# Optimization experiments

Hardware: AMD Instinct MI355X
Metric: run time of the kernel (lower is better)

The kernel has to match this reference:

```python
import jax, jax.numpy as jnp
import numpy as np

H = 8
D_MODEL = 1024
DIM_G = 64
WAVE_LEN = 1000.0


def box_relational_embedding(f_g):
    # f_g: [B, N, 4] -> [B, N, N, 64] trigonometric geometry embedding
    B, N, _ = f_g.shape
    x_min, y_min, x_max, y_max = jnp.split(f_g, 4, axis=-1)  # each [B, N, 1]
    cx = (x_min + x_max) * 0.5
    cy = (y_min + y_max) * 0.5
    w = x_max - x_min + 1.0
    h = y_max - y_min + 1.0
    # row i vs column j deltas, normalized by row box size
    dx = jnp.log(jnp.maximum(jnp.abs((cx - cx.reshape(B, 1, N)) / w), 1e-3))
    dy = jnp.log(jnp.maximum(jnp.abs((cy - cy.reshape(B, 1, N)) / h), 1e-3))
    dw = jnp.log(w / w.reshape(B, 1, N))
    dh = jnp.log(h / h.reshape(B, 1, N))
    pos = jnp.stack([dx, dy, dw, dh], axis=-1)  # [B, N, N, 4]
    feat_range = jnp.arange(DIM_G // 8, dtype=jnp.float32) / (DIM_G / 8.0)
    dim_mat = 1.0 / jnp.power(WAVE_LEN, feat_range)  # [8]
    mul = (100.0 * pos)[..., None] * dim_mat  # [B, N, N, 4, 8]
    mul = mul.reshape(B, N, N, DIM_G // 2)
    return jnp.concatenate([jnp.sin(mul), jnp.cos(mul)], axis=-1)  # [B, N, N, 64]


def setup_inputs() -> dict:
    key = jax.random.key(0)
    ks = jax.random.split(key, 12)
    B, N, D = 16, 256, D_MODEL
    q = jax.random.normal(ks[0], (B, N, D), jnp.float32)
    k = jax.random.normal(ks[1], (B, N, D), jnp.float32)
    v = jax.random.normal(ks[2], (B, N, D), jnp.float32)
    # valid boxes: x_max > x_min, y_max > y_min
    xy = jax.random.uniform(ks[3], (B, N, 2), jnp.float32) * 100.0
    wh = jax.random.uniform(ks[4], (B, N, 2), jnp.float32) * 50.0 + 1.0
    input_box = jnp.concatenate([xy, xy + wh], axis=-1)  # [B, N, 4]
    s = 0.02
    Wq = jax.random.normal(ks[5], (D, D), jnp.float32) * s
    Wk = jax.random.normal(ks[6], (D, D), jnp.float32) * s
    Wv = jax.random.normal(ks[7], (D, D), jnp.float32) * s
    Wo = jax.random.normal(ks[8], (D, D), jnp.float32) * s
    bq = jnp.zeros((D,), jnp.float32)
    bk = jnp.zeros((D,), jnp.float32)
    bv = jnp.zeros((D,), jnp.float32)
    bo = jnp.zeros((D,), jnp.float32)
    Wg = jax.random.normal(ks[9], (H, DIM_G), jnp.float32) * 0.1  # stacked per-head Linear(64,1)
    bg = jax.random.normal(ks[10], (H,), jnp.float32) * 0.1
    return {"input_query": q, "input_key": k, "input_value": v, "input_box": input_box,
            "Wq": Wq, "bq": bq, "Wk": Wk, "bk": bk, "Wv": Wv, "bv": bv,
            "Wg": Wg, "bg": bg, "Wo": Wo, "bo": bo}


def reference(input_query, input_key, input_value, input_box,
              Wq, bq, Wk, bk, Wv, bv, Wg, bg, Wo, bo):
    B, N, D = input_query.shape
    d_k = D // H

    def proj(x, W, b):
        return (x @ W + b).reshape(B, N, H, d_k).transpose(0, 2, 1, 3)  # [B,H,N,dk]

    q = proj(input_query, Wq, bq)
    k = proj(input_key, Wk, bk)
    v = proj(input_value, Wv, bv)

    emb = box_relational_embedding(input_box)  # [B, N, N, 64]
    # per-head Linear(64 -> 1), stacked: [B, H, N, N]
    rel_w = jax.nn.relu(jnp.einsum('bmng,hg->bhmn', emb, Wg) + bg[None, :, None, None])

    scores = jnp.einsum('bhqd,bhkd->bhqk', q, k) / np.sqrt(d_k).astype(np.float32)
    logits = jnp.log(jnp.maximum(rel_w, 1e-6)) + scores
    attn = jax.nn.softmax(logits, axis=-1)  # [B, H, N, N]
    out = jnp.einsum('bhqk,bhkd->bhqd', attn, v)
    out = out.transpose(0, 2, 1, 3).reshape(B, N, D)
    return out @ Wo + bo
```

## Files before the change

### kernel.cpp

```cpp
#include <hip/hip_runtime.h>
#include <hip/hip_bf16.h>
#include <hip/hip_fp16.h>
#include <math.h>

#define B_  16
#define N_  256
#define D_  1024
#define H_  8
#define DK_ 128

typedef unsigned short u16;
typedef __attribute__((ext_vector_type(8))) short s8v;
typedef __attribute__((ext_vector_type(4))) float f4v;

__device__ __forceinline__ u16 f2b(float x) {
    union { float f; unsigned u; } v; v.f = x;
    unsigned r = v.u + 0x7fffu + ((v.u >> 16) & 1u);
    return (u16)(r >> 16);
}

__device__ __forceinline__ void gload16(void* lds, const void* g) {
    __builtin_amdgcn_global_load_lds(
        (const __attribute__((address_space(1))) void*)g,
        (__attribute__((address_space(3))) void*)lds, 16, 0, 0);
}

__device__ __forceinline__ void waitv8() { asm volatile("s_waitcnt vmcnt(8)" ::: "memory"); }
__device__ __forceinline__ void waitv6() { asm volatile("s_waitcnt vmcnt(6)" ::: "memory"); }
__device__ __forceinline__ void waitv4() { asm volatile("s_waitcnt vmcnt(4)" ::: "memory"); }
__device__ __forceinline__ void waitv3() { asm volatile("s_waitcnt vmcnt(3)" ::: "memory"); }
__device__ __forceinline__ void waitv0() { asm volatile("s_waitcnt vmcnt(0)" ::: "memory"); }
__device__ __forceinline__ void membar() { asm volatile("" ::: "memory"); }

__global__ __launch_bounds__(256)
void cvt_kernel(const float* __restrict__ x0, const float* __restrict__ x1,
                const float* __restrict__ x2, u16* __restrict__ out)
{
    const float* in = (blockIdx.y == 0) ? x0 : (blockIdx.y == 1) ? x1 : x2;
    u16* o = out + (size_t)blockIdx.y * 4194304;
    const int i = blockIdx.x * 256 + threadIdx.x;
    const float4 a = ((const float4*)in)[2 * i];
    const float4 b = ((const float4*)in)[2 * i + 1];
    union { u16 s[8]; uint4 v; } t;
    t.s[0] = f2b(a.x); t.s[1] = f2b(a.y); t.s[2] = f2b(a.z); t.s[3] = f2b(a.w);
    t.s[4] = f2b(b.x); t.s[5] = f2b(b.y); t.s[6] = f2b(b.z); t.s[7] = f2b(b.w);
    ((uint4*)o)[i] = t.v;
}

__global__ __launch_bounds__(256)
void cvtT_kernel(const float* __restrict__ W0, const float* __restrict__ W1,
                 const float* __restrict__ W2, const float* __restrict__ W3,
                 u16* __restrict__ out)
{
    const float* W = (blockIdx.z == 0) ? W0 : (blockIdx.z == 1) ? W1 :
                     (blockIdx.z == 2) ? W2 : W3;
    u16* o = out + (size_t)blockIdx.z * (D_ * D_);
    __shared__ float t[32][33];
    const int k0 = blockIdx.x * 32, n0 = blockIdx.y * 32;
    const int c = threadIdx.x & 31, r8 = threadIdx.x >> 5;
#pragma unroll
    for (int rr = 0; rr < 4; ++rr)
        t[r8 + rr * 8][c] = W[(size_t)(k0 + r8 + rr * 8) * D_ + n0 + c];
    __syncthreads();
#pragma unroll
    for (int rr = 0; rr < 4; ++rr)
        o[(size_t)(n0 + r8 + rr * 8) * D_ + k0 + c] = f2b(t[c][r8 + rr * 8]);
}

template<int BM, int FM, int LOADS, int MODE>
__global__ __launch_bounds__(256)
void gemm_kernel(const u16* __restrict__ A0, const u16* __restrict__ Wt0,
                 const float* __restrict__ b0, const float* __restrict__ b1,
                 const float* __restrict__ b2, void* __restrict__ outb)
{
    constexpr int WM  = FM * 16;
    constexpr int MT8 = (4096 / BM) / 8;
    __shared__ __align__(16) u16 As[3][BM][32];
    __shared__ __align__(16) u16 Bs[3][128][32];

    const int z = blockIdx.z;
    const u16* A  = A0  + (size_t)z * 4194304;
    const u16* Wt = Wt0 + (size_t)z * 1048576;
    const float* bias = (z == 0) ? b0 : (z == 1) ? b1 : b2;

    const int bid = blockIdx.x;
    const int xcd = bid & 7;
    const int wic = bid >> 3;
    const int by  = xcd * MT8 + (wic & (MT8 - 1));
    const int bx  = wic / MT8;
    const int m0  = by * BM;
    const int n0  = bx * 128;

    const int tid  = threadIdx.x;
    const int lane = tid & 63;
    const int w    = tid >> 6;
    const int l15  = lane & 15;
    const int l4   = lane >> 4;
    const int wr   = w >> 1;
    const int wc   = w & 1;

    const int gr   = tid >> 2;
    const int c4   = tid & 3;
    const int scol = (c4 ^ ((gr >> 1) & 3)) * 8;
    const int doff = c4 * 8;
    const u16* asrc = A  + (size_t)(m0 + gr) * 1024 + scol;
    const u16* bsrc = Wt + (size_t)(n0 + gr) * 1024 + scol;
    const int fc = (l4 ^ ((l15 >> 1) & 3)) * 8;

    auto stage = [&](int buf, int kt) {
        const int k0_ = kt * 32;
        gload16(&As[buf][gr][doff], asrc + k0_);
        if constexpr (BM == 128)
            gload16(&As[buf][gr + 64][doff], asrc + 64 * 1024 + k0_);
        gload16(&Bs[buf][gr][doff], bsrc + k0_);
        gload16(&Bs[buf][gr + 64][doff], bsrc + 64 * 1024 + k0_);
    };

    f4v acc[FM][4] = {};

    stage(0, 0);
    stage(1, 1);
    int cur = 0, stg = 2;

    for (int kt = 0; kt < 32; ++kt) {
        membar();
        __builtin_amdgcn_s_barrier();
        if (kt < 30) {
            stage(stg, kt + 2);
            if constexpr (LOADS == 4) waitv8(); else waitv6();
        } else if (kt == 30) {
            if constexpr (LOADS == 4) waitv4(); else waitv3();
        } else {
            waitv0();
        }
        membar();
        __builtin_amdgcn_s_barrier();

        s8v af[FM], bf[4];
#pragma unroll
        for (int i = 0; i < FM; ++i)
            af[i] = *(const s8v*)&As[cur][wr * WM + i * 16 + l15][fc];
#pragma unroll
        for (int j = 0; j < 4; ++j)
            bf[j] = *(const s8v*)&Bs[cur][wc * 64 + j * 16 + l15][fc];
#pragma unroll
        for (int i = 0; i < FM; ++i)
#pragma unroll
            for (int j = 0; j < 4; ++j)
                acc[i][j] = __builtin_amdgcn_mfma_f32_16x16x32_bf16(
                    af[i], bf[j], acc[i][j], 0, 0, 0);

        cur = (cur == 2) ? 0 : cur + 1;
        stg = (stg == 2) ? 0 : stg + 1;
    }

#pragma unroll
    for (int j = 0; j < 4; ++j) {
        const int n = n0 + wc * 64 + j * 16 + l15;
        const float bb = bias[n];
#pragma unroll
        for (int i = 0; i < FM; ++i) {
            const int mbase = m0 + wr * WM + i * 16 + l4 * 4;
            if constexpr (MODE == 0) {
#pragma unroll
                for (int reg = 0; reg < 4; ++reg)
                    ((float*)outb)[(size_t)(mbase + reg) * 1024 + n] =
                        acc[i][j][reg] + bb;
            } else {
                if (z == 2) {
                    const int b = mbase >> 8, tok = mbase & 255;
                    const int h = n >> 7, d = n & 127;
                    ushort4 st;
                    st.x = f2b(acc[i][j][0] + bb);
                    st.y = f2b(acc[i][j][1] + bb);
                    st.z = f2b(acc[i][j][2] + bb);
                    st.w = f2b(acc[i][j][3] + bb);
                    *(ushort4*)&((u16*)outb)[(size_t)z * 4194304 +
                        (((size_t)b * H_ + h) * DK_ + d) * N_ + tok] = st;
                } else {
                    const int h = n >> 7, d = n & 127;
#pragma unroll
                    for (int reg = 0; reg < 4; ++reg) {
                        const int m = mbase + reg;
                        const int b = m >> 8, tok = m & 255;
                        ((u16*)outb)[(size_t)z * 4194304 +
                            (((size_t)b * H_ + h) * N_ + tok) * DK_ + d] =
                            f2b(acc[i][j][reg] + bb);
                    }
                }
            }
        }
    }
}

__global__ __launch_bounds__(256)
void boxbias_kernel(const float* __restrict__ fg, const float* __restrict__ Wg,
                    const float* __restrict__ bg, _Float16* __restrict__ lb)
{
    __shared__ float sWg[512];
    __shared__ float sbg[8];
    const int tid = threadIdx.x;
    const int b = blockIdx.x >> 8;
    const int i = blockIdx.x & 255;

    sWg[tid] = Wg[tid];
    sWg[tid + 256] = Wg[tid + 256];
    if (tid < 8) sbg[tid] = bg[tid];

    const float4 bi = *(const float4*)&fg[(size_t)(b * N_ + i) * 4];
    const float cxi = 0.5f * (bi.x + bi.z);
    const float cyi = 0.5f * (bi.y + bi.w);
    const float wi  = bi.z - bi.x + 1.0f;
    const float hi  = bi.w - bi.y + 1.0f;

    const int j = tid;
    const float4 bj = *(const float4*)&fg[(size_t)(b * N_ + j) * 4];
    const float cxj = 0.5f * (bj.x + bj.z);
    const float cyj = 0.5f * (bj.y + bj.w);
    const float wj  = bj.z - bj.x + 1.0f;
    const float hj  = bj.w - bj.y + 1.0f;

    const float pos[4] = {
        logf(fmaxf(fabsf((cxi - cxj) / wi), 1e-3f)) * 100.0f,
        logf(fmaxf(fabsf((cyi - cyj) / hi), 1e-3f)) * 100.0f,
        logf(wi / wj) * 100.0f,
        logf(hi / hj) * 100.0f
    };
    const float dim[8] = {1.0f, 0.421696503f, 0.177827941f, 0.0749894209f,
                          0.0316227766f, 0.0133352143f, 0.00562341325f, 0.00237137371f};

    float sv[32], cv[32];
#pragma unroll
    for (int p = 0; p < 4; ++p)
#pragma unroll
        for (int q = 0; q < 8; ++q)
            __sincosf(pos[p] * dim[q], &sv[p * 8 + q], &cv[p * 8 + q]);

    __syncthreads();
#pragma unroll
    for (int h = 0; h < 8; ++h) {
        float acc = sbg[h];
        const float* wrow = &sWg[h * 64];
#pragma unroll
        for (int g = 0; g < 32; ++g)
            acc = fmaf(sv[g], wrow[g], fmaf(cv[g], wrow[32 + g], acc));
        const float rel = fmaxf(acc, 0.0f);
        lb[(((size_t)b * H_ + h) * N_ + i) * N_ + j] =
            (_Float16)logf(fmaxf(rel, 1e-6f));
    }
}

__global__ __launch_bounds__(256)
void attn_mfma_kernel(const u16* __restrict__ qp, const u16* __restrict__ kp,
                      const u16* __restrict__ vp, const _Float16* __restrict__ lb,
                      u16* __restrict__ ao)
{
    __shared__ __align__(16) u16 Ks[32][136];
    __shared__ __align__(16) u16 Vt[128][40];
    __shared__ __align__(16) u16 Ps[4][32][40];

    const int tid  = threadIdx.x;
    const int lane = tid & 63;
    const int w    = tid >> 6;
    const int l15  = lane & 15;
    const int l4   = lane >> 4;
    const int bh   = blockIdx.x >> 1;
    const int qt   = blockIdx.x & 1;
    const int q0   = qt * 128 + w * 32;

    s8v qf[2][4];
    const u16* qb = qp + ((size_t)bh * N_ + q0) * DK_;
#pragma unroll
    for (int mf = 0; mf < 2; ++mf)
#pragma unroll
        for (int ks = 0; ks < 4; ++ks)
            qf[mf][ks] = *(const s8v*)(qb + (size_t)(mf * 16 + l15) * DK_ + ks * 32 + l4 * 8);

    f4v o[2][8] = {};
    float m_r[2][4], l_r[2][4];
#pragma unroll
    for (int mf = 0; mf < 2; ++mf)
#pragma unroll
        for (int r = 0; r < 4; ++r) { m_r[mf][r] = -INFINITY; l_r[mf][r] = 0.0f; }

    const float scale = 0.08838834764831845f;
    const _Float16* lbb = lb + ((size_t)bh * N_ + q0) * N_;

    const int sr = tid >> 3;
    const int sc = (tid & 7) * 16;
    const int vr = tid >> 2;
    const int vs = (tid & 3) * 8;

    for (int kt = 0; kt < 8; ++kt) {
        __syncthreads();
        {
            const u16* ksrc = kp + ((size_t)bh * N_ + kt * 32) * DK_;
            *(s8v*)&Ks[sr][sc]     = *(const s8v*)(ksrc + (size_t)sr * DK_ + sc);
            *(s8v*)&Ks[sr][sc + 8] = *(const s8v*)(ksrc + (size_t)sr * DK_ + sc + 8);
        }
        {
            const u16* vsrc = vp + ((size_t)bh * DK_ + vr) * N_ + kt * 32 + vs;
            const s8v v0 = *(const s8v*)vsrc;
            const s8v v1 = *(const s8v*)(vsrc + 64 * N_);
            *(s8v*)&Vt[vr][vs]      = v0;
            *(s8v*)&Vt[vr + 64][vs] = v1;
        }
        __syncthreads();

        f4v s[2][2] = {};
#pragma unroll
        for (int ks = 0; ks < 4; ++ks) {
#pragma unroll
            for (int kf = 0; kf < 2; ++kf) {
                const s8v kb = *(const s8v*)&Ks[kf * 16 + l15][ks * 32 + l4 * 8];
#pragma unroll
                for (int mf = 0; mf < 2; ++mf)
                    s[mf][kf] = __builtin_amdgcn_mfma_f32_16x16x32_bf16(
                        qf[mf][ks], kb, s[mf][kf], 0, 0, 0);
            }
        }
#pragma unroll
        for (int mf = 0; mf < 2; ++mf)
#pragma unroll
            for (int kf = 0; kf < 2; ++kf)
#pragma unroll
                for (int r = 0; r < 4; ++r)
                    s[mf][kf][r] = fmaf(s[mf][kf][r], scale, (float)
                        lbb[(size_t)(mf * 16 + l4 * 4 + r) * N_ + kt * 32 + kf * 16 + l15]);

#pragma unroll
        for (int mf = 0; mf < 2; ++mf) {
            float rm[4], al[4];
#pragma unroll
            for (int r = 0; r < 4; ++r) rm[r] = fmaxf(s[mf][0][r], s[mf][1][r]);
#pragma unroll
            for (int st = 1; st <= 8; st <<= 1)
#pragma unroll
                for (int r = 0; r < 4; ++r) rm[r] = fmaxf(rm[r], __shfl_xor(rm[r], st));
#pragma unroll
            for (int r = 0; r < 4; ++r) {
                const float mn = fmaxf(m_r[mf][r], rm[r]);
                al[r] = __expf(m_r[mf][r] - mn);
                m_r[mf][r] = mn;
            }
            float p0[4], p1[4], rs[4];
#pragma unroll
            for (int r = 0; r < 4; ++r) {
                p0[r] = __expf(s[mf][0][r] - m_r[mf][r]);
                p1[r] = __expf(s[mf][1][r] - m_r[mf][r]);
                rs[r] = p0[r] + p1[r];
            }
#pragma unroll
            for (int st = 1; st <= 8; st <<= 1)
#pragma unroll
                for (int r = 0; r < 4; ++r) rs[r] += __shfl_xor(rs[r], st);
#pragma unroll
            for (int r = 0; r < 4; ++r) {
                l_r[mf][r] = l_r[mf][r] * al[r] + rs[r];
                Ps[w][mf * 16 + l4 * 4 + r][l15]      = f2b(p0[r]);
                Ps[w][mf * 16 + l4 * 4 + r][16 + l15] = f2b(p1[r]);
            }
#pragma unroll
            for (int nf = 0; nf < 8; ++nf)
#pragma unroll
                for (int r = 0; r < 4; ++r) o[mf][nf][r] *= al[r];
        }

        s8v pa[2];
#pragma unroll
        for (int mf = 0; mf < 2; ++mf)
            pa[mf] = *(const s8v*)&Ps[w][mf * 16 + l15][l4 * 8];
#pragma unroll
        for (int nf = 0; nf < 8; ++nf) {
            const s8v vb = *(const s8v*)&Vt[nf * 16 + l15][l4 * 8];
#pragma unroll
            for (int mf = 0; mf < 2; ++mf)
                o[mf][nf] = __builtin_amdgcn_mfma_f32_16x16x32_bf16(
                    pa[mf], vb, o[mf][nf], 0, 0, 0);
        }
    }

    const int b = bh >> 3, h = bh & 7;
#pragma unroll
    for (int mf = 0; mf < 2; ++mf) {
        float inv[4];
#pragma unroll
        for (int r = 0; r < 4; ++r) inv[r] = 1.0f / l_r[mf][r];
#pragma unroll
        for (int nf = 0; nf < 8; ++nf) {
#pragma unroll
            for (int r = 0; r < 4; ++r) {
                const int tok = q0 + mf * 16 + l4 * 4 + r;
                const int d = nf * 16 + l15;
                ao[(((size_t)b * N_ + tok) * H_ + h) * DK_ + d] = f2b(o[mf][nf][r] * inv[r]);
            }
        }
    }
}

extern "C" void kernel_launch(void* const* d_in, const int* in_sizes, int n_in,
                              void* d_out, int out_size, void* d_ws, size_t ws_size,
                              hipStream_t stream)
{
    const float* xq = (const float*)d_in[0];
    const float* xk = (const float*)d_in[1];
    const float* xv = (const float*)d_in[2];
    const float* fg = (const float*)d_in[3];
    const float* Wq = (const float*)d_in[4];
    const float* bq = (const float*)d_in[5];
    const float* Wk = (const float*)d_in[6];
    const float* bk = (const float*)d_in[7];
    const float* Wv = (const float*)d_in[8];
    const float* bv = (const float*)d_in[9];
    const float* Wg = (const float*)d_in[10];
    const float* bg = (const float*)d_in[11];
    const float* Wo = (const float*)d_in[12];
    const float* bo = (const float*)d_in[13];

    char* w8 = (char*)d_ws;
    u16*      xb  = (u16*)(w8);
    u16*      Wt  = (u16*)(w8 + 25165824);
    u16*      qkv = (u16*)(w8 + 33554432);
    _Float16* lb  = (_Float16*)(w8 + 58720256);
    u16*      ao  = (u16*)(w8 + 75497472);

    cvt_kernel<<<dim3(2048, 3), 256, 0, stream>>>(xq, xk, xv, xb);
    cvtT_kernel<<<dim3(32, 32, 4), 256, 0, stream>>>(Wq, Wk, Wv, Wo, Wt);

    gemm_kernel<128, 4, 4, 1><<<dim3(256, 1, 3), 256, 0, stream>>>(
        xb, Wt, bq, bk, bv, qkv);

    boxbias_kernel<<<B_ * N_, 256, 0, stream>>>(fg, Wg, bg, lb);

    attn_mfma_kernel<<<B_ * H_ * 2, 256, 0, stream>>>(
        qkv, qkv + 4194304, qkv + 2 * 4194304, lb, ao);

    gemm_kernel<64, 2, 3, 0><<<dim3(512, 1, 1), 256, 0, stream>>>(
        ao, Wt + 3 * 1048576, bo, bo, bo, d_out);
}
```

Baseline: 128.3 us.

## Merge prep and box-bias launches, split attention into 64-row query tiles

```diff
diff --git a/kernel.cpp b/kernel.cpp
--- a/kernel.cpp
+++ b/kernel.cpp
@@ -33,140 +33,136 @@
 __device__ __forceinline__ void membar() { asm volatile("" ::: "memory"); }
 
 __global__ __launch_bounds__(256)
-void cvt_kernel(const float* __restrict__ x0, const float* __restrict__ x1,
-                const float* __restrict__ x2, u16* __restrict__ out)
+void prep_kernel(const float* __restrict__ x0, const float* __restrict__ x1,
+                 const float* __restrict__ x2,
+                 const float* __restrict__ W0, const float* __restrict__ W1,
+                 const float* __restrict__ W2, const float* __restrict__ W3,
+                 u16* __restrict__ xb, u16* __restrict__ Wt)
 {
-    const float* in = (blockIdx.y == 0) ? x0 : (blockIdx.y == 1) ? x1 : x2;
-    u16* o = out + (size_t)blockIdx.y * 4194304;
-    const int i = blockIdx.x * 256 + threadIdx.x;
-    const float4 a = ((const float4*)in)[2 * i];
-    const float4 b = ((const float4*)in)[2 * i + 1];
-    union { u16 s[8]; uint4 v; } t;
-    t.s[0] = f2b(a.x); t.s[1] = f2b(a.y); t.s[2] = f2b(a.z); t.s[3] = f2b(a.w);
-    t.s[4] = f2b(b.x); t.s[5] = f2b(b.y); t.s[6] = f2b(b.z); t.s[7] = f2b(b.w);
-    ((uint4*)o)[i] = t.v;
+    const int bx = blockIdx.x;
+    if (bx < 6144) {
+        const int y = bx >> 11;
+        const float* in = (y == 0) ? x0 : (y == 1) ? x1 : x2;
+        u16* o = xb + (size_t)y * 4194304;
+        const int i = (bx & 2047) * 256 + threadIdx.x;
+        const float4 a = ((const float4*)in)[2 * i];
+        const float4 b = ((const float4*)in)[2 * i + 1];
+        union { u16 s[8]; uint4 v; } t;
+        t.s[0] = f2b(a.x); t.s[1] = f2b(a.y); t.s[2] = f2b(a.z); t.s[3] = f2b(a.w);
+        t.s[4] = f2b(b.x); t.s[5] = f2b(b.y); t.s[6] = f2b(b.z); t.s[7] = f2b(b.w);
+        ((uint4*)o)[i] = t.v;
+    } else {
+        __shared__ float t[32][33];
+        const int tt = bx - 6144;
+        const int z  = tt >> 10;
+        const int rem = tt & 1023;
+        const int k0 = (rem & 31) * 32;
+        const int n0 = (rem >> 5) * 32;
+        const float* W = (z == 0) ? W0 : (z == 1) ? W1 : (z == 2) ? W2 : W3;
+        u16* o = Wt + (size_t)z * (D_ * D_);
+        const int c = threadIdx.x & 31, r8 = threadIdx.x >> 5;
+#pragma unroll
+        for (int rr = 0; rr < 4; ++rr)
+            t[r8 + rr * 8][c] = W[(size_t)(k0 + r8 + rr * 8) * D_ + n0 + c];
+        __syncthreads();
+#pragma unroll
+        for (int rr = 0; rr < 4; ++rr)
+            o[(size_t)(n0 + r8 + rr * 8) * D_ + k0 + c] = f2b(t[c][r8 + rr * 8]);
+    }
 }
 
 __global__ __launch_bounds__(256)
-void cvtT_kernel(const float* __restrict__ W0, const float* __restrict__ W1,
-                 const float* __restrict__ W2, const float* __restrict__ W3,
-                 u16* __restrict__ out)
+void qkv_boxbias_kernel(const u16* __restrict__ A0, const u16* __restrict__ Wt0,
+                        const float* __restrict__ b0, const float* __restrict__ b1,
+                        const float* __restrict__ b2, u16* __restrict__ qkv,
+                        const float* __restrict__ fg, const float* __restrict__ Wg,
+                        const float* __restrict__ bg, _Float16* __restrict__ lb)
 {
-    const float* W = (blockIdx.z == 0) ? W0 : (blockIdx.z == 1) ? W1 :
-                     (blockIdx.z == 2) ? W2 : W3;
-    u16* o = out + (size_t)blockIdx.z * (D_ * D_);
-    __shared__ float t[32][33];
-    const int k0 = blockIdx.x * 32, n0 = blockIdx.y * 32;
-    const int c = threadIdx.x & 31, r8 = threadIdx.x >> 5;
-#pragma unroll
-    for (int rr = 0; rr < 4; ++rr)
-        t[r8 + rr * 8][c] = W[(size_t)(k0 + r8 + rr * 8) * D_ + n0 + c];
-    __syncthreads();
-#pragma unroll
-    for (int rr = 0; rr < 4; ++rr)
-        o[(size_t)(n0 + r8 + rr * 8) * D_ + k0 + c] = f2b(t[c][r8 + rr * 8]);
-}
-
-template<int BM, int FM, int LOADS, int MODE>
-__global__ __launch_bounds__(256)
-void gemm_kernel(const u16* __restrict__ A0, const u16* __restrict__ Wt0,
-                 const float* __restrict__ b0, const float* __restrict__ b1,
-                 const float* __restrict__ b2, void* __restrict__ outb)
-{
-    constexpr int WM  = FM * 16;
-    constexpr int MT8 = (4096 / BM) / 8;
-    __shared__ __align__(16) u16 As[3][BM][32];
+    __shared__ __align__(16) u16 As[3][128][32];
     __shared__ __align__(16) u16 Bs[3][128][32];
-
-    const int z = blockIdx.z;
-    const u16* A  = A0  + (size_t)z * 4194304;
-    const u16* Wt = Wt0 + (size_t)z * 1048576;
-    const float* bias = (z == 0) ? b0 : (z == 1) ? b1 : b2;
-
-    const int bid = blockIdx.x;
-    const int xcd = bid & 7;
-    const int wic = bid >> 3;
-    const int by  = xcd * MT8 + (wic & (MT8 - 1));
-    const int bx  = wic / MT8;
-    const int m0  = by * BM;
-    const int n0  = bx * 128;
-
-    const int tid  = threadIdx.x;
-    const int lane = tid & 63;
-    const int w    = tid >> 6;
-    const int l15  = lane & 15;
-    const int l4   = lane >> 4;
-    const int wr   = w >> 1;
-    const int wc   = w & 1;
-
-    const int gr   = tid >> 2;
-    const int c4   = tid & 3;
-    const int scol = (c4 ^ ((gr >> 1) & 3)) * 8;
-    const int doff = c4 * 8;
-    const u16* asrc = A  + (size_t)(m0 + gr) * 1024 + scol;
-    const u16* bsrc = Wt + (size_t)(n0 + gr) * 1024 + scol;
-    const int fc = (l4 ^ ((l15 >> 1) & 3)) * 8;
-
-    auto stage = [&](int buf, int kt) {
-        const int k0_ = kt * 32;
-        gload16(&As[buf][gr][doff], asrc + k0_);
-        if constexpr (BM == 128)
+    __shared__ float sWg[512];
+    __shared__ float sbg[8];
+
+    const int tid = threadIdx.x;
+
+    if (blockIdx.x < 768) {
+        const int gbx = blockIdx.x;
+        const int z   = gbx >> 8;
+        const int bid = gbx & 255;
+        const u16* A  = A0  + (size_t)z * 4194304;
+        const u16* Wt = Wt0 + (size_t)z * 1048576;
+        const float* bias = (z == 0) ? b0 : (z == 1) ? b1 : b2;
+
+        const int xcd = bid & 7;
+        const int wic = bid >> 3;
+        const int by  = xcd * 4 + (wic & 3);
+        const int bx_ = wic >> 2;
+        const int m0  = by * 128;
+        const int n0  = bx_ * 128;
+
+        const int lane = tid & 63;
+        const int w    = tid >> 6;
+        const int l15  = lane & 15;
+        const int l4   = lane >> 4;
+        const int wr   = w >> 1;
+        const int wc   = w & 1;
+
+        const int gr   = tid >> 2;
+        const int c4   = tid & 3;
+        const int scol = (c4 ^ ((gr >> 1) & 3)) * 8;
+        const int doff = c4 * 8;
+        const u16* asrc = A  + (size_t)(m0 + gr) * 1024 + scol;
+        const u16* bsrc = Wt + (size_t)(n0 + gr) * 1024 + scol;
+        const int fc = (l4 ^ ((l15 >> 1) & 3)) * 8;
+
+        auto stage = [&](int buf, int kt) {
+            const int k0_ = kt * 32;
+            gload16(&As[buf][gr][doff],      asrc + k0_);
             gload16(&As[buf][gr + 64][doff], asrc + 64 * 1024 + k0_);
-        gload16(&Bs[buf][gr][doff], bsrc + k0_);
-        gload16(&Bs[buf][gr + 64][doff], bsrc + 64 * 1024 + k0_);
-    };
-
-    f4v acc[FM][4] = {};
-
-    stage(0, 0);
-    stage(1, 1);
-    int cur = 0, stg = 2;
-
-    for (int kt = 0; kt < 32; ++kt) {
-        membar();
-        __builtin_amdgcn_s_barrier();
-        if (kt < 30) {
-            stage(stg, kt + 2);
-            if constexpr (LOADS == 4) waitv8(); else waitv6();
-        } else if (kt == 30) {
-            if constexpr (LOADS == 4) waitv4(); else waitv3();
-        } else {
-            waitv0();
-        }
-        membar();
-        __builtin_amdgcn_s_barrier();
-
-        s8v af[FM], bf[4];
-#pragma unroll
-        for (int i = 0; i < FM; ++i)
-            af[i] = *(const s8v*)&As[cur][wr * WM + i * 16 + l15][fc];
-#pragma unroll
-        for (int j = 0; j < 4; ++j)
-            bf[j] = *(const s8v*)&Bs[cur][wc * 64 + j * 16 + l15][fc];
-#pragma unroll
-        for (int i = 0; i < FM; ++i)
+            gload16(&Bs[buf][gr][doff],      bsrc + k0_);
+            gload16(&Bs[buf][gr + 64][doff], bsrc + 64 * 1024 + k0_);
+        };
+
+        f4v acc[4][4] = {};
+
+        stage(0, 0);
+        stage(1, 1);
+        int cur = 0, stg = 2;
+
+        for (int kt = 0; kt < 32; ++kt) {
+            membar();
+            __builtin_amdgcn_s_barrier();
+            if (kt < 30) { stage(stg, kt + 2); waitv8(); }
+            else if (kt == 30) { waitv4(); }
+            else { waitv0(); }
+            membar();
+            __builtin_amdgcn_s_barrier();
+
+            s8v af[4], bf[4];
+#pragma unroll
+            for (int i = 0; i < 4; ++i)
+                af[i] = *(const s8v*)&As[cur][wr * 64 + i * 16 + l15][fc];
 #pragma unroll
             for (int j = 0; j < 4; ++j)
-                acc[i][j] = __builtin_amdgcn_mfma_f32_16x16x32_bf16(
-                    af[i], bf[j], acc[i][j], 0, 0, 0);
-
-        cur = (cur == 2) ? 0 : cur + 1;
-        stg = (stg == 2) ? 0 : stg + 1;
-    }
-
-#pragma unroll
-    for (int j = 0; j < 4; ++j) {
-        const int n = n0 + wc * 64 + j * 16 + l15;
-        const float bb = bias[n];
-#pragma unroll
-        for (int i = 0; i < FM; ++i) {
-            const int mbase = m0 + wr * WM + i * 16 + l4 * 4;
-            if constexpr (MODE == 0) {
-#pragma unroll
-                for (int reg = 0; reg < 4; ++reg)
-                    ((float*)outb)[(size_t)(mbase + reg) * 1024 + n] =
-                        acc[i][j][reg] + bb;
-            } else {
+                bf[j] = *(const s8v*)&Bs[cur][wc * 64 + j * 16 + l15][fc];
+#pragma unroll
+            for (int i = 0; i < 4; ++i)
+#pragma unroll
+                for (int j = 0; j < 4; ++j)
+                    acc[i][j] = __builtin_amdgcn_mfma_f32_16x16x32_bf16(
+                        af[i], bf[j], acc[i][j], 0, 0, 0);
+
+            cur = (cur == 2) ? 0 : cur + 1;
+            stg = (stg == 2) ? 0 : stg + 1;
+        }
+
+#pragma unroll
+        for (int j = 0; j < 4; ++j) {
+            const int n = n0 + wc * 64 + j * 16 + l15;
+            const float bb = bias[n];
+#pragma unroll
+            for (int i = 0; i < 4; ++i) {
+                const int mbase = m0 + wr * 64 + i * 16 + l4 * 4;
                 if (z == 2) {
                     const int b = mbase >> 8, tok = mbase & 255;
                     const int h = n >> 7, d = n & 127;
@@ -175,7 +171,7 @@
                     st.y = f2b(acc[i][j][1] + bb);
                     st.z = f2b(acc[i][j][2] + bb);
                     st.w = f2b(acc[i][j][3] + bb);
-                    *(ushort4*)&((u16*)outb)[(size_t)z * 4194304 +
+                    *(ushort4*)&qkv[(size_t)z * 4194304 +
                         (((size_t)b * H_ + h) * DK_ + d) * N_ + tok] = st;
                 } else {
                     const int h = n >> 7, d = n & 127;
@@ -183,70 +179,148 @@
                     for (int reg = 0; reg < 4; ++reg) {
                         const int m = mbase + reg;
                         const int b = m >> 8, tok = m & 255;
-                        ((u16*)outb)[(size_t)z * 4194304 +
+                        qkv[(size_t)z * 4194304 +
                             (((size_t)b * H_ + h) * N_ + tok) * DK_ + d] =
                             f2b(acc[i][j][reg] + bb);
                     }
                 }
             }
         }
+    } else {
+        const int bb = blockIdx.x - 768;
+        const int b = bb >> 8;
+        const int i = bb & 255;
+
+        sWg[tid] = Wg[tid];
+        sWg[tid + 256] = Wg[tid + 256];
+        if (tid < 8) sbg[tid] = bg[tid];
+
+        const float4 bi = *(const float4*)&fg[(size_t)(b * N_ + i) * 4];
+        const float cxi = 0.5f * (bi.x + bi.z);
+        const float cyi = 0.5f * (bi.y + bi.w);
+        const float wi  = bi.z - bi.x + 1.0f;
+        const float hi  = bi.w - bi.y + 1.0f;
+
+        const int j = tid;
+        const float4 bj = *(const float4*)&fg[(size_t)(b * N_ + j) * 4];
+        const float cxj = 0.5f * (bj.x + bj.z);
+        const float cyj = 0.5f * (bj.y + bj.w);
+        const float wj  = bj.z - bj.x + 1.0f;
+        const float hj  = bj.w - bj.y + 1.0f;
+
+        const float pos[4] = {
+            logf(fmaxf(fabsf((cxi - cxj) / wi), 1e-3f)) * 100.0f,
+            logf(fmaxf(fabsf((cyi - cyj) / hi), 1e-3f)) * 100.0f,
+            logf(wi / wj) * 100.0f,
+            logf(hi / hj) * 100.0f
+        };
+        const float dim[8] = {1.0f, 0.421696503f, 0.177827941f, 0.0749894209f,
+                              0.0316227766f, 0.0133352143f, 0.00562341325f, 0.00237137371f};
+
+        float sv[32], cv[32];
+#pragma unroll
+        for (int p = 0; p < 4; ++p)
+#pragma unroll
+            for (int q = 0; q < 8; ++q)
+                __sincosf(pos[p] * dim[q], &sv[p * 8 + q], &cv[p * 8 + q]);
+
+        __syncthreads();
+#pragma unroll
+        for (int h = 0; h < 8; ++h) {
+            float acc = sbg[h];
+            const float* wrow = &sWg[h * 64];
+#pragma unroll
+            for (int g = 0; g < 32; ++g)
+                acc = fmaf(sv[g], wrow[g], fmaf(cv[g], wrow[32 + g], acc));
+            const float rel = fmaxf(acc, 0.0f);
+            lb[(((size_t)b * H_ + h) * N_ + i) * N_ + j] =
+                (_Float16)logf(fmaxf(rel, 1e-6f));
+        }
     }
 }
 
 __global__ __launch_bounds__(256)
-void boxbias_kernel(const float* __restrict__ fg, const float* __restrict__ Wg,
-                    const float* __restrict__ bg, _Float16* __restrict__ lb)
+void gemm_out_kernel(const u16* __restrict__ A, const u16* __restrict__ Wt,
+                     const float* __restrict__ bias, float* __restrict__ outb)
 {
-    __shared__ float sWg[512];
-    __shared__ float sbg[8];
-    const int tid = threadIdx.x;
-    const int b = blockIdx.x >> 8;
-    const int i = blockIdx.x & 255;
-
-    sWg[tid] = Wg[tid];
-    sWg[tid + 256] = Wg[tid + 256];
-    if (tid < 8) sbg[tid] = bg[tid];
-
-    const float4 bi = *(const float4*)&fg[(size_t)(b * N_ + i) * 4];
-    const float cxi = 0.5f * (bi.x + bi.z);
-    const float cyi = 0.5f * (bi.y + bi.w);
-    const float wi  = bi.z - bi.x + 1.0f;
-    const float hi  = bi.w - bi.y + 1.0f;
-
-    const int j = tid;
-    const float4 bj = *(const float4*)&fg[(size_t)(b * N_ + j) * 4];
-    const float cxj = 0.5f * (bj.x + bj.z);
-    const float cyj = 0.5f * (bj.y + bj.w);
-    const float wj  = bj.z - bj.x + 1.0f;
-    const float hj  = bj.w - bj.y + 1.0f;
-
-    const float pos[4] = {
-        logf(fmaxf(fabsf((cxi - cxj) / wi), 1e-3f)) * 100.0f,
-        logf(fmaxf(fabsf((cyi - cyj) / hi), 1e-3f)) * 100.0f,
-        logf(wi / wj) * 100.0f,
-        logf(hi / hj) * 100.0f
+    __shared__ __align__(16) u16 As[3][64][32];
+    __shared__ __align__(16) u16 Bs[3][128][32];
+
+    const int bid = blockIdx.x;
+    const int xcd = bid & 7;
+    const int wic = bid >> 3;
+    const int by  = xcd * 8 + (wic & 7);
+    const int bx  = wic >> 3;
+    const int m0  = by * 64;
+    const int n0  = bx * 128;
+
+    const int tid  = threadIdx.x;
+    const int lane = tid & 63;
+    const int w    = tid >> 6;
+    const int l15  = lane & 15;
+    const int l4   = lane >> 4;
+    const int wr   = w >> 1;
+    const int wc   = w & 1;
+
+    const int gr   = tid >> 2;
+    const int c4   = tid & 3;
+    const int scol = (c4 ^ ((gr >> 1) & 3)) * 8;
+    const int doff = c4 * 8;
+    const u16* asrc = A  + (size_t)(m0 + gr) * 1024 + scol;
+    const u16* bsrc = Wt + (size_t)(n0 + gr) * 1024 + scol;
+    const int fc = (l4 ^ ((l15 >> 1) & 3)) * 8;
+
+    auto stage = [&](int buf, int kt) {
+        const int k0_ = kt * 32;
+        gload16(&As[buf][gr & 63][doff], asrc + k0_);
+        gload16(&Bs[buf][gr][doff],      bsrc + k0_);
+        gload16(&Bs[buf][gr + 64][doff], bsrc + 64 * 1024 + k0_);
     };
-    const float dim[8] = {1.0f, 0.421696503f, 0.177827941f, 0.0749894209f,
-                          0.0316227766f, 0.0133352143f, 0.00562341325f, 0.00237137371f};
-
-    float sv[32], cv[32];
-#pragma unroll
-    for (int p = 0; p < 4; ++p)
-#pragma unroll
-        for (int q = 0; q < 8; ++q)
-            __sincosf(pos[p] * dim[q], &sv[p * 8 + q], &cv[p * 8 + q]);
-
-    __syncthreads();
-#pragma unroll
-    for (int h = 0; h < 8; ++h) {
-        float acc = sbg[h];
-        const float* wrow = &sWg[h * 64];
-#pragma unroll
-        for (int g = 0; g < 32; ++g)
-            acc = fmaf(sv[g], wrow[g], fmaf(cv[g], wrow[32 + g], acc));
-        const float rel = fmaxf(acc, 0.0f);
-        lb[(((size_t)b * H_ + h) * N_ + i) * N_ + j] =
-            (_Float16)logf(fmaxf(rel, 1e-6f));
+
+    f4v acc[2][4] = {};
+
+    stage(0, 0);
+    stage(1, 1);
+    int cur = 0, stg = 2;
+
+    for (int kt = 0; kt < 32; ++kt) {
+        membar();
+        __builtin_amdgcn_s_barrier();
+        if (kt < 30) { stage(stg, kt + 2); waitv6(); }
+        else if (kt == 30) { waitv3(); }
+        else { waitv0(); }
+        membar();
+        __builtin_amdgcn_s_barrier();
+
+        s8v af[2], bf[4];
+#pragma unroll
+        for (int i = 0; i < 2; ++i)
+            af[i] = *(const s8v*)&As[cur][wr * 32 + i * 16 + l15][fc];
+#pragma unroll
+        for (int j = 0; j < 4; ++j)
+            bf[j] = *(const s8v*)&Bs[cur][wc * 64 + j * 16 + l15][fc];
+#pragma unroll
+        for (int i = 0; i < 2; ++i)
+#pragma unroll
+            for (int j = 0; j < 4; ++j)
+                acc[i][j] = __builtin_amdgcn_mfma_f32_16x16x32_bf16(
+                    af[i], bf[j], acc[i][j], 0, 0, 0);
+
+        cur = (cur == 2) ? 0 : cur + 1;
+        stg = (stg == 2) ? 0 : stg + 1;
+    }
+
+#pragma unroll
+    for (int j = 0; j < 4; ++j) {
+        const int n = n0 + wc * 64 + j * 16 + l15;
+        const float bb = bias[n];
+#pragma unroll
+        for (int i = 0; i < 2; ++i) {
+            const int mbase = m0 + wr * 32 + i * 16 + l4 * 4;
+#pragma unroll
+            for (int reg = 0; reg < 4; ++reg)
+                outb[(size_t)(mbase + reg) * 1024 + n] = acc[i][j][reg] + bb;
+        }
     }
 }
 
@@ -257,31 +331,27 @@
 {
     __shared__ __align__(16) u16 Ks[32][136];
     __shared__ __align__(16) u16 Vt[128][40];
-    __shared__ __align__(16) u16 Ps[4][32][40];
+    __shared__ __align__(16) u16 Ps[4][16][40];
 
     const int tid  = threadIdx.x;
     const int lane = tid & 63;
     const int w    = tid >> 6;
     const int l15  = lane & 15;
     const int l4   = lane >> 4;
-    const int bh   = blockIdx.x >> 1;
-    const int qt   = blockIdx.x & 1;
-    const int q0   = qt * 128 + w * 32;
-
-    s8v qf[2][4];
+    const int bh   = blockIdx.x >> 2;
+    const int qt   = blockIdx.x & 3;
+    const int q0   = qt * 64 + w * 16;
+
+    s8v qf[4];
     const u16* qb = qp + ((size_t)bh * N_ + q0) * DK_;
 #pragma unroll
-    for (int mf = 0; mf < 2; ++mf)
-#pragma unroll
-        for (int ks = 0; ks < 4; ++ks)
-            qf[mf][ks] = *(const s8v*)(qb + (size_t)(mf * 16 + l15) * DK_ + ks * 32 + l4 * 8);
-
-    f4v o[2][8] = {};
-    float m_r[2][4], l_r[2][4];
-#pragma unroll
-    for (int mf = 0; mf < 2; ++mf)
-#pragma unroll
-        for (int r = 0; r < 4; ++r) { m_r[mf][r] = -INFINITY; l_r[mf][r] = 0.0f; }
+    for (int ks = 0; ks < 4; ++ks)
+        qf[ks] = *(const s8v*)(qb + (size_t)l15 * DK_ + ks * 32 + l4 * 8);
+
+    f4v o[8] = {};
+    float m_r[4], l_r[4];
+#pragma unroll
+    for (int r = 0; r < 4; ++r) { m_r[r] = -INFINITY; l_r[r] = 0.0f; }
 
     const float scale = 0.08838834764831845f;
     const _Float16* lbb = lb + ((size_t)bh * N_ + q0) * N_;
@@ -307,47 +377,42 @@
         }
         __syncthreads();
 
-        f4v s[2][2] = {};
+        f4v s[2] = {};
 #pragma unroll
         for (int ks = 0; ks < 4; ++ks) {
 #pragma unroll
             for (int kf = 0; kf < 2; ++kf) {
                 const s8v kb = *(const s8v*)&Ks[kf * 16 + l15][ks * 32 + l4 * 8];
-#pragma unroll
-                for (int mf = 0; mf < 2; ++mf)
-                    s[mf][kf] = __builtin_amdgcn_mfma_f32_16x16x32_bf16(
-                        qf[mf][ks], kb, s[mf][kf], 0, 0, 0);
+                s[kf] = __builtin_amdgcn_mfma_f32_16x16x32_bf16(
+                    qf[ks], kb, s[kf], 0, 0, 0);
             }
         }
 #pragma unroll
-        for (int mf = 0; mf < 2; ++mf)
-#pragma unroll
-            for (int kf = 0; kf < 2; ++kf)
-#pragma unroll
-                for (int r = 0; r < 4; ++r)
-                    s[mf][kf][r] = fmaf(s[mf][kf][r], scale, (float)
-                        lbb[(size_t)(mf * 16 + l4 * 4 + r) * N_ + kt * 32 + kf * 16 + l15]);
-
-#pragma unroll
-        for (int mf = 0; mf < 2; ++mf) {
+        for (int kf = 0; kf < 2; ++kf)
+#pragma unroll
+            for (int r = 0; r < 4; ++r)
+                s[kf][r] = fmaf(s[kf][r], scale, (float)
+                    lbb[(size_t)(l4 * 4 + r) * N_ + kt * 32 + kf * 16 + l15]);
+
+        {
             float rm[4], al[4];
 #pragma unroll
-            for (int r = 0; r < 4; ++r) rm[r] = fmaxf(s[mf][0][r], s[mf][1][r]);
+            for (int r = 0; r < 4; ++r) rm[r] = fmaxf(s[0][r], s[1][r]);
 #pragma unroll
             for (int st = 1; st <= 8; st <<= 1)
 #pragma unroll
                 for (int r = 0; r < 4; ++r) rm[r] = fmaxf(rm[r], __shfl_xor(rm[r], st));
 #pragma unroll
             for (int r = 0; r < 4; ++r) {
-                const float mn = fmaxf(m_r[mf][r], rm[r]);
-                al[r] = __expf(m_r[mf][r] - mn);
-                m_r[mf][r] = mn;
+                const float mn = fmaxf(m_r[r], rm[r]);
+                al[r] = __expf(m_r[r] - mn);
+                m_r[r] = mn;
             }
             float p0[4], p1[4], rs[4];
 #pragma unroll
             for (int r = 0; r < 4; ++r) {
-                p0[r] = __expf(s[mf][0][r] - m_r[mf][r]);
-                p1[r] = __expf(s[mf][1][r] - m_r[mf][r]);
+                p0[r] = __expf(s[0][r] - m_r[r]);
+                p1[r] = __expf(s[1][r] - m_r[r]);
                 rs[r] = p0[r] + p1[r];
             }
 #pragma unroll
@@ -356,44 +421,35 @@
                 for (int r = 0; r < 4; ++r) rs[r] += __shfl_xor(rs[r], st);
 #pragma unroll
             for (int r = 0; r < 4; ++r) {
-                l_r[mf][r] = l_r[mf][r] * al[r] + rs[r];
-                Ps[w][mf * 16 + l4 * 4 + r][l15]      = f2b(p0[r]);
-                Ps[w][mf * 16 + l4 * 4 + r][16 + l15] = f2b(p1[r]);
+                l_r[r] = l_r[r] * al[r] + rs[r];
+                Ps[w][l4 * 4 + r][l15]      = f2b(p0[r]);
+                Ps[w][l4 * 4 + r][16 + l15] = f2b(p1[r]);
             }
 #pragma unroll
             for (int nf = 0; nf < 8; ++nf)
 #pragma unroll
-                for (int r = 0; r < 4; ++r) o[mf][nf][r] *= al[r];
-        }
-
-        s8v pa[2];
-#pragma unroll
-        for (int mf = 0; mf < 2; ++mf)
-            pa[mf] = *(const s8v*)&Ps[w][mf * 16 + l15][l4 * 8];
+                for (int r = 0; r < 4; ++r) o[nf][r] *= al[r];
+        }
+
+        const s8v pa = *(const s8v*)&Ps[w][l15][l4 * 8];
 #pragma unroll
         for (int nf = 0; nf < 8; ++nf) {
             const s8v vb = *(const s8v*)&Vt[nf * 16 + l15][l4 * 8];
-#pragma unroll
-            for (int mf = 0; mf < 2; ++mf)
-                o[mf][nf] = __builtin_amdgcn_mfma_f32_16x16x32_bf16(
-                    pa[mf], vb, o[mf][nf], 0, 0, 0);
+            o[nf] = __builtin_amdgcn_mfma_f32_16x16x32_bf16(pa, vb, o[nf], 0, 0, 0);
         }
     }
 
     const int b = bh >> 3, h = bh & 7;
-#pragma unroll
-    for (int mf = 0; mf < 2; ++mf) {
-        float inv[4];
-#pragma unroll
-        for (int r = 0; r < 4; ++r) inv[r] = 1.0f / l_r[mf][r];
-#pragma unroll
-        for (int nf = 0; nf < 8; ++nf) {
-#pragma unroll
-            for (int r = 0; r < 4; ++r) {
-                const int tok = q0 + mf * 16 + l4 * 4 + r;
-                const int d = nf * 16 + l15;
-                ao[(((size_t)b * N_ + tok) * H_ + h) * DK_ + d] = f2b(o[mf][nf][r] * inv[r]);
-            }
+    float inv[4];
+#pragma unroll
+    for (int r = 0; r < 4; ++r) inv[r] = 1.0f / l_r[r];
+#pragma unroll
+    for (int nf = 0; nf < 8; ++nf) {
+#pragma unroll
+        for (int r = 0; r < 4; ++r) {
+            const int tok = q0 + l4 * 4 + r;
+            const int d = nf * 16 + l15;
+            ao[(((size_t)b * N_ + tok) * H_ + h) * DK_ + d] = f2b(o[nf][r] * inv[r]);
         }
     }
 }
@@ -424,17 +480,14 @@
     _Float16* lb  = (_Float16*)(w8 + 58720256);
     u16*      ao  = (u16*)(w8 + 75497472);
 
-    cvt_kernel<<<dim3(2048, 3), 256, 0, stream>>>(xq, xk, xv, xb);
-    cvtT_kernel<<<dim3(32, 32, 4), 256, 0, stream>>>(Wq, Wk, Wv, Wo, Wt);
-
-    gemm_kernel<128, 4, 4, 1><<<dim3(256, 1, 3), 256, 0, stream>>>(
-        xb, Wt, bq, bk, bv, qkv);
-
-    boxbias_kernel<<<B_ * N_, 256, 0, stream>>>(fg, Wg, bg, lb);
-
-    attn_mfma_kernel<<<B_ * H_ * 2, 256, 0, stream>>>(
+    prep_kernel<<<10240, 256, 0, stream>>>(xq, xk, xv, Wq, Wk, Wv, Wo, xb, Wt);
+
+    qkv_boxbias_kernel<<<768 + 4096, 256, 0, stream>>>(
+        xb, Wt, bq, bk, bv, qkv, fg, Wg, bg, lb);
+
+    attn_mfma_kernel<<<512, 256, 0, stream>>>(
         qkv, qkv + 4194304, qkv + 2 * 4194304, lb, ao);
 
-    gemm_kernel<64, 2, 3, 0><<<dim3(512, 1, 1), 256, 0, stream>>>(
-        ao, Wt + 3 * 1048576, bo, bo, bo, d_out);
-}
+    gemm_out_kernel<<<512, 256, 0, stream>>>(
+        ao, Wt + 3 * 1048576, bo, (float*)d_out);
+}
```

After: 132.8 us. 3.5% more time.

## Split attention into 16-row wave tiles across 512 blocks; vectorize box-bias weight loads

Applied to the files above, without the earlier changes.

```diff
diff --git a/kernel.cpp b/kernel.cpp
--- a/kernel.cpp
+++ b/kernel.cpp
@@ -197,7 +197,7 @@
 void boxbias_kernel(const float* __restrict__ fg, const float* __restrict__ Wg,
                     const float* __restrict__ bg, _Float16* __restrict__ lb)
 {
-    __shared__ float sWg[512];
+    __shared__ __align__(16) float sWg[512];
     __shared__ float sbg[8];
     const int tid = threadIdx.x;
     const int b = blockIdx.x >> 8;
@@ -242,8 +242,14 @@
         float acc = sbg[h];
         const float* wrow = &sWg[h * 64];
 #pragma unroll
-        for (int g = 0; g < 32; ++g)
-            acc = fmaf(sv[g], wrow[g], fmaf(cv[g], wrow[32 + g], acc));
+        for (int g0 = 0; g0 < 32; g0 += 4) {
+            const float4 ws = *(const float4*)&wrow[g0];
+            const float4 wc = *(const float4*)&wrow[32 + g0];
+            acc = fmaf(sv[g0 + 0], ws.x, fmaf(cv[g0 + 0], wc.x, acc));
+            acc = fmaf(sv[g0 + 1], ws.y, fmaf(cv[g0 + 1], wc.y, acc));
+            acc = fmaf(sv[g0 + 2], ws.z, fmaf(cv[g0 + 2], wc.z, acc));
+            acc = fmaf(sv[g0 + 3], ws.w, fmaf(cv[g0 + 3], wc.w, acc));
+        }
         const float rel = fmaxf(acc, 0.0f);
         lb[(((size_t)b * H_ + h) * N_ + i) * N_ + j] =
             (_Float16)logf(fmaxf(rel, 1e-6f));
@@ -257,31 +263,27 @@
 {
     __shared__ __align__(16) u16 Ks[32][136];
     __shared__ __align__(16) u16 Vt[128][40];
-    __shared__ __align__(16) u16 Ps[4][32][40];
+    __shared__ __align__(16) u16 Ps[4][16][40];
 
     const int tid  = threadIdx.x;
     const int lane = tid & 63;
     const int w    = tid >> 6;
     const int l15  = lane & 15;
     const int l4   = lane >> 4;
-    const int bh   = blockIdx.x >> 1;
-    const int qt   = blockIdx.x & 1;
-    const int q0   = qt * 128 + w * 32;
-
-    s8v qf[2][4];
+    const int bh   = blockIdx.x >> 2;
+    const int qt   = blockIdx.x & 3;
+    const int q0   = qt * 64 + w * 16;
+
+    s8v qf[4];
     const u16* qb = qp + ((size_t)bh * N_ + q0) * DK_;
 #pragma unroll
-    for (int mf = 0; mf < 2; ++mf)
-#pragma unroll
-        for (int ks = 0; ks < 4; ++ks)
-            qf[mf][ks] = *(const s8v*)(qb + (size_t)(mf * 16 + l15) * DK_ + ks * 32 + l4 * 8);
-
-    f4v o[2][8] = {};
-    float m_r[2][4], l_r[2][4];
-#pragma unroll
-    for (int mf = 0; mf < 2; ++mf)
-#pragma unroll
-        for (int r = 0; r < 4; ++r) { m_r[mf][r] = -INFINITY; l_r[mf][r] = 0.0f; }
+    for (int ks = 0; ks < 4; ++ks)
+        qf[ks] = *(const s8v*)(qb + (size_t)l15 * DK_ + ks * 32 + l4 * 8);
+
+    f4v o[8] = {};
+    float m_r[4], l_r[4];
+#pragma unroll
+    for (int r = 0; r < 4; ++r) { m_r[r] = -INFINITY; l_r[r] = 0.0f; }
 
     const float scale = 0.08838834764831845f;
     const _Float16* lbb = lb + ((size_t)bh * N_ + q0) * N_;
@@ -307,47 +309,42 @@
         }
         __syncthreads();
 
-        f4v s[2][2] = {};
+        f4v s[2] = {};
 #pragma unroll
         for (int ks = 0; ks < 4; ++ks) {
 #pragma unroll
             for (int kf = 0; kf < 2; ++kf) {
                 const s8v kb = *(const s8v*)&Ks[kf * 16 + l15][ks * 32 + l4 * 8];
-#pragma unroll
-                for (int mf = 0; mf < 2; ++mf)
-                    s[mf][kf] = __builtin_amdgcn_mfma_f32_16x16x32_bf16(
-                        qf[mf][ks], kb, s[mf][kf], 0, 0, 0);
+                s[kf] = __builtin_amdgcn_mfma_f32_16x16x32_bf16(
+                    qf[ks], kb, s[kf], 0, 0, 0);
             }
         }
 #pragma unroll
-        for (int mf = 0; mf < 2; ++mf)
-#pragma unroll
-            for (int kf = 0; kf < 2; ++kf)
-#pragma unroll
-                for (int r = 0; r < 4; ++r)
-                    s[mf][kf][r] = fmaf(s[mf][kf][r], scale, (float)
-                        lbb[(size_t)(mf * 16 + l4 * 4 + r) * N_ + kt * 32 + kf * 16 + l15]);
-
-#pragma unroll
-        for (int mf = 0; mf < 2; ++mf) {
+        for (int kf = 0; kf < 2; ++kf)
+#pragma unroll
+            for (int r = 0; r < 4; ++r)
+                s[kf][r] = fmaf(s[kf][r], scale, (float)
+                    lbb[(size_t)(l4 * 4 + r) * N_ + kt * 32 + kf * 16 + l15]);
+
+        {
             float rm[4], al[4];
 #pragma unroll
-            for (int r = 0; r < 4; ++r) rm[r] = fmaxf(s[mf][0][r], s[mf][1][r]);
+            for (int r = 0; r < 4; ++r) rm[r] = fmaxf(s[0][r], s[1][r]);
 #pragma unroll
             for (int st = 1; st <= 8; st <<= 1)
 #pragma unroll
                 for (int r = 0; r < 4; ++r) rm[r] = fmaxf(rm[r], __shfl_xor(rm[r], st));
 #pragma unroll
             for (int r = 0; r < 4; ++r) {
-                const float mn = fmaxf(m_r[mf][r], rm[r]);
-                al[r] = __expf(m_r[mf][r] - mn);
-                m_r[mf][r] = mn;
+                const float mn = fmaxf(m_r[r], rm[r]);
+                al[r] = __expf(m_r[r] - mn);
+                m_r[r] = mn;
             }
             float p0[4], p1[4], rs[4];
 #pragma unroll
             for (int r = 0; r < 4; ++r) {
-                p0[r] = __expf(s[mf][0][r] - m_r[mf][r]);
-                p1[r] = __expf(s[mf][1][r] - m_r[mf][r]);
+                p0[r] = __expf(s[0][r] - m_r[r]);
+                p1[r] = __expf(s[1][r] - m_r[r]);
                 rs[r] = p0[r] + p1[r];
             }
 #pragma unroll
@@ -356,44 +353,35 @@
                 for (int r = 0; r < 4; ++r) rs[r] += __shfl_xor(rs[r], st);
 #pragma unroll
             for (int r = 0; r < 4; ++r) {
-                l_r[mf][r] = l_r[mf][r] * al[r] + rs[r];
-                Ps[w][mf * 16 + l4 * 4 + r][l15]      = f2b(p0[r]);
-                Ps[w][mf * 16 + l4 * 4 + r][16 + l15] = f2b(p1[r]);
+                l_r[r] = l_r[r] * al[r] + rs[r];
+                Ps[w][l4 * 4 + r][l15]      = f2b(p0[r]);
+                Ps[w][l4 * 4 + r][16 + l15] = f2b(p1[r]);
             }
 #pragma unroll
             for (int nf = 0; nf < 8; ++nf)
 #pragma unroll
-                for (int r = 0; r < 4; ++r) o[mf][nf][r] *= al[r];
-        }
-
-        s8v pa[2];
-#pragma unroll
-        for (int mf = 0; mf < 2; ++mf)
-            pa[mf] = *(const s8v*)&Ps[w][mf * 16 + l15][l4 * 8];
+                for (int r = 0; r < 4; ++r) o[nf][r] *= al[r];
+        }
+
+        const s8v pa = *(const s8v*)&Ps[w][l15][l4 * 8];
 #pragma unroll
         for (int nf = 0; nf < 8; ++nf) {
             const s8v vb = *(const s8v*)&Vt[nf * 16 + l15][l4 * 8];
-#pragma unroll
-            for (int mf = 0; mf < 2; ++mf)
-                o[mf][nf] = __builtin_amdgcn_mfma_f32_16x16x32_bf16(
-                    pa[mf], vb, o[mf][nf], 0, 0, 0);
+            o[nf] = __builtin_amdgcn_mfma_f32_16x16x32_bf16(pa, vb, o[nf], 0, 0, 0);
         }
     }
 
     const int b = bh >> 3, h = bh & 7;
-#pragma unroll
-    for (int mf = 0; mf < 2; ++mf) {
-        float inv[4];
-#pragma unroll
-        for (int r = 0; r < 4; ++r) inv[r] = 1.0f / l_r[mf][r];
-#pragma unroll
-        for (int nf = 0; nf < 8; ++nf) {
-#pragma unroll
-            for (int r = 0; r < 4; ++r) {
-                const int tok = q0 + mf * 16 + l4 * 4 + r;
-                const int d = nf * 16 + l15;
-                ao[(((size_t)b * N_ + tok) * H_ + h) * DK_ + d] = f2b(o[mf][nf][r] * inv[r]);
-            }
+    float inv[4];
+#pragma unroll
+    for (int r = 0; r < 4; ++r) inv[r] = 1.0f / l_r[r];
+#pragma unroll
+    for (int nf = 0; nf < 8; ++nf) {
+#pragma unroll
+        for (int r = 0; r < 4; ++r) {
+            const int tok = q0 + l4 * 4 + r;
+            const int d = nf * 16 + l15;
+            ao[(((size_t)b * N_ + tok) * H_ + h) * DK_ + d] = f2b(o[nf][r] * inv[r]);
         }
     }
 }
@@ -432,7 +420,7 @@
 
     boxbias_kernel<<<B_ * N_, 256, 0, stream>>>(fg, Wg, bg, lb);
 
-    attn_mfma_kernel<<<B_ * H_ * 2, 256, 0, stream>>>(
+    attn_mfma_kernel<<<512, 256, 0, stream>>>(
         qkv, qkv + 4194304, qkv + 2 * 4194304, lb, ao);
 
     gemm_kernel<64, 2, 3, 0><<<dim3(512, 1, 1), 256, 0, stream>>>(
```

Result: no change. 126.6 us (-1.3%).
